# Performance work log

Hardware: AMD Instinct MI355X
Metric: run time of the kernel (lower is better)

The kernel has to match this reference:

```python
import jax, jax.numpy as jnp
import numpy as np

MODES1, MODES2 = 32, 32

def fht_matrix(N):
    # Exact linear-operator form of the repo's recursive fht1d (N must be a power of two,
    # which it is here, so the pad/truncate branch never triggers).
    if N == 1:
        return np.ones((1, 1), np.float32)
    M = fht_matrix(N // 2)
    k = np.arange(N // 2)
    cas = (np.cos(2 * np.pi * k / N) + np.sin(2 * np.pi * k / N)).astype(np.float32)[:, None]
    E = np.zeros((N // 2, N), np.float32); E[:, 0::2] = M   # even-index sub-transform
    O = np.zeros((N // 2, N), np.float32); O[:, 1::2] = M   # odd-index sub-transform
    return np.concatenate([E + cas * O, E - cas * O], axis=0)

def dht2(x, M1, M2):
    # apply the (pseudo-)Hartley transform along dims 2 then 3: X[k,l] = sum_{h,w} M1[k,h] M2[l,w] x[h,w]
    return jnp.einsum('bchw,kh,lw->bckl', x, M1, M2)

def neg_freq(a):
    # index map k -> (-k mod m) on the last two dims (flip then roll by 1)
    return jnp.roll(jnp.flip(a, axis=(-2, -1)), shift=(1, 1), axis=(-2, -1))

def compl_mul2d(x1, x2):
    x1n = neg_freq(x1)
    x2n = neg_freq(x2)
    return 0.5 * (jnp.einsum('bixy,ioxy->boxy', x1, x2)
                  - jnp.einsum('bixy,ioxy->boxy', x1n, x2n)
                  + jnp.einsum('bixy,ioxy->boxy', x1, x2n)
                  + jnp.einsum('bixy,ioxy->boxy', x1n, x2))

def setup_inputs() -> dict:
    key = jax.random.key(0)
    k1, k2 = jax.random.split(key)
    B, Cin, Cout, S = 32, 64, 64, 128
    x = jax.random.normal(k1, (B, Cin, S, S), jnp.float32)
    scale = 1.0 / (Cin * Cout)
    weights1 = scale * jax.random.uniform(k2, (Cin, Cout, MODES1, MODES2), jnp.float32)
    return {"x": x, "weights1": weights1}

def reference(x, weights1):
    B, Cin, S1, S2 = x.shape
    Cout = weights1.shape[1]
    M1 = jnp.asarray(fht_matrix(S1))
    M2 = jnp.asarray(fht_matrix(S2))
    x_ht = dht2(x, M1, M2)                                        # [B,Cin,S1,S2]
    block = compl_mul2d(x_ht[:, :, :MODES1, :MODES2], weights1)   # [B,Cout,m1,m2]
    out_ht = jnp.zeros((B, Cout, S1, S2), x.dtype).at[:, :, :MODES1, :MODES2].set(block)
    # idht = dht / (S1*S2)
    return dht2(out_ht, M1, M2) / (S1 * S2)
```

## Files before the change

### kernel.cpp

```cpp
#include <hip/hip_runtime.h>
#include <math.h>


#define SS   128
#define MD   32
#define NBAT 32
#define CI   64
#define CO   64

#define TWO_PI 6.2831853071795864769

typedef __attribute__((ext_vector_type(8))) short bf16x8;
typedef __attribute__((ext_vector_type(4))) float f32x4;

static const size_t OFF_XH   = 32768;
static const size_t OFF_XHT  = 32768 + 2097152;
static const size_t OFF_WT   = 32768 + 2 * 2097152;
static const size_t OFF_BLKT = OFF_XH;
static const size_t OFF_BLK  = OFF_XHT;
static const size_t OFF_MFH  = OFF_WT + 4194304;
static const size_t OFF_MFL  = OFF_MFH + 8192;

__device__ inline float m_entry(int k, int n) {
    float prod = 1.f;
    int kk = k, nn = n;
    for (int Nj = SS; Nj > 1; Nj >>= 1) {
        int half = Nj >> 1;
        int k1 = kk & (half - 1);
        if (nn & 1) {
            double ang = (TWO_PI / (double)Nj) * (double)k1;
            float cas = (float)(cos(ang) + sin(ang));
            prod *= (kk < half) ? cas : -cas;
        }
        kk = k1;
        nn >>= 1;
    }
    return prod;
}

__device__ inline unsigned short f2bf(float f) {
    unsigned u = __float_as_uint(f);
    return (unsigned short)((u + 0x7FFF + ((u >> 16) & 1)) >> 16);
}
__device__ inline float bf2f(unsigned short h) {
    return __uint_as_float((unsigned)h << 16);
}
__device__ inline void split2(float a, float b, unsigned& hi, unsigned& lo) {
    unsigned short ah = f2bf(a), bh = f2bf(b);
    hi = (unsigned)ah | ((unsigned)bh << 16);
    lo = (unsigned)f2bf(a - bf2f(ah)) | ((unsigned)f2bf(b - bf2f(bh)) << 16);
}
__device__ inline void fsplit2(float a, float b, unsigned& hi, unsigned& lo) {
    unsigned ua = __float_as_uint(a), ub = __float_as_uint(b);
    unsigned ha = (ua + 0x8000u) & 0xFFFF0000u;
    unsigned hb = (ub + 0x8000u) & 0xFFFF0000u;
    float la = a - __uint_as_float(ha);
    float lb = b - __uint_as_float(hb);
    hi = (ha >> 16) | hb;
    lo = (__float_as_uint(la) >> 16) | (__float_as_uint(lb) & 0xFFFF0000u);
}
__device__ inline bf16x8 pack4(unsigned a, unsigned b, unsigned c, unsigned d) {
    union { unsigned u[4]; bf16x8 v; } w;
    w.u[0] = a; w.u[1] = b; w.u[2] = c; w.u[3] = d;
    return w.v;
}

__global__ __launch_bounds__(256) void k_prep(const float* __restrict__ wgt,
                                              float* __restrict__ Wt,
                                              unsigned short* __restrict__ MFH,
                                              unsigned short* __restrict__ MFL) {
    const int bid = blockIdx.x;
    const int t   = threadIdx.x;
    if (bid >= 4096) {
        int idx2 = (bid - 4096) * 256 + t;
        int j    = idx2 & 7;
        int lane = (idx2 >> 3) & 63;
        int s    = (idx2 >> 9) & 3;
        int tt   = idx2 >> 11;
        int kq   = tt * 16 + (lane & 15);
        int nq   = s * 32 + ((lane >> 4) << 3) + j;
        float f  = m_entry(kq, nq);
        unsigned short hi = f2bf(f);
        MFH[idx2] = hi;
        MFL[idx2] = f2bf(f - bf2f(hi));
        return;
    }
    __shared__ float tile[32][33];
    const int mt  = bid & 31;
    const int iot = bid >> 5;
    const int tx = t & 31;
    const int ty = t >> 5;
#pragma unroll
    for (int j = 0; j < 4; ++j) {
        int r = ty + 8 * j;
        tile[r][tx] = wgt[(iot * 32 + r) * 1024 + mt * 32 + tx];
    }
    __syncthreads();
#pragma unroll
    for (int j = 0; j < 4; ++j) {
        int r = ty + 8 * j;
        Wt[(mt * 32 + r) * 4096 + iot * 32 + tx] = tile[tx][r];
    }
}

__global__ __launch_bounds__(256, 3) void k_fwd4(const float* __restrict__ x,
                                                 const unsigned short* __restrict__ MFH,
                                                 const unsigned short* __restrict__ MFL,
                                                 float* __restrict__ Xh) {
    const int bc = blockIdx.x;
    const float* xp = x + (size_t)bc * 16384;
    const int t = threadIdx.x;
    const int lane = t & 63, wid = t >> 6;
    const int l15 = lane & 15, g = lane >> 4;

    __shared__ unsigned short Ybf[2][32 * 136];

    const int hbase = wid * 32;
    const int ra = (hbase + l15) * 128 + g * 8;
    const int rb = (hbase + 16 + l15) * 128 + g * 8;

    float4 xall[4][2][2];
#pragma unroll
    for (int s = 0; s < 4; ++s) {
        xall[s][0][0] = *(const float4*)(xp + ra + s * 32);
        xall[s][0][1] = *(const float4*)(xp + ra + s * 32 + 4);
        xall[s][1][0] = *(const float4*)(xp + rb + s * 32);
        xall[s][1][1] = *(const float4*)(xp + rb + s * 32 + 4);
    }

    f32x4 acc[2][2] = {};

#pragma unroll
    for (int s = 0; s < 4; ++s) {
        bf16x8 Bh[2], Bl[2];
#pragma unroll
        for (int lt = 0; lt < 2; ++lt) {
            const int bidx = (lt * 4 + s) * 64 + lane;
            Bh[lt] = ((const bf16x8*)MFH)[bidx];
            Bl[lt] = ((const bf16x8*)MFL)[bidx];
        }
#pragma unroll
        for (int hh = 0; hh < 2; ++hh) {
            const float4 v0 = xall[s][hh][0];
            const float4 v1 = xall[s][hh][1];
            unsigned h0, l0, h1, l1, h2, l2, h3, l3;
            fsplit2(v0.x, v0.y, h0, l0);
            fsplit2(v0.z, v0.w, h1, l1);
            fsplit2(v1.x, v1.y, h2, l2);
            fsplit2(v1.z, v1.w, h3, l3);
            const bf16x8 Ah = pack4(h0, h1, h2, h3);
            const bf16x8 Al = pack4(l0, l1, l2, l3);
#pragma unroll
            for (int lt = 0; lt < 2; ++lt) {
                acc[hh][lt] = __builtin_amdgcn_mfma_f32_16x16x32_bf16(Ah, Bh[lt], acc[hh][lt], 0, 0, 0);
                acc[hh][lt] = __builtin_amdgcn_mfma_f32_16x16x32_bf16(Ah, Bl[lt], acc[hh][lt], 0, 0, 0);
                acc[hh][lt] = __builtin_amdgcn_mfma_f32_16x16x32_bf16(Al, Bh[lt], acc[hh][lt], 0, 0, 0);
            }
        }
    }

#pragma unroll
    for (int hh = 0; hh < 2; ++hh) {
#pragma unroll
        for (int lt = 0; lt < 2; ++lt) {
            int lmode = lt * 16 + l15;
            int h0 = hbase + hh * 16 + g * 4;
            f32x4 v = acc[hh][lt];
            unsigned hi01, lo01, hi23, lo23;
            split2(v[0], v[1], hi01, lo01);
            split2(v[2], v[3], hi23, lo23);
            ((uint2*)&Ybf[0][0])[lmode * 34 + (h0 >> 2)] = make_uint2(hi01, hi23);
            ((uint2*)&Ybf[1][0])[lmode * 34 + (h0 >> 2)] = make_uint2(lo01, lo23);
        }
    }
    __syncthreads();

    const int kt = wid >> 1, lt2 = wid & 1;
    f32x4 z = {};
#pragma unroll
    for (int s2 = 0; s2 < 4; ++s2) {
        int aidx = (kt * 4 + s2) * 64 + lane;
        bf16x8 Ah = ((const bf16x8*)MFH)[aidx];
        bf16x8 Al = ((const bf16x8*)MFL)[aidx];
        int lmode = lt2 * 16 + l15;
        int yidx = lmode * 17 + s2 * 4 + g;
        bf16x8 Yh = ((const bf16x8*)&Ybf[0][0])[yidx];
        bf16x8 Yl = ((const bf16x8*)&Ybf[1][0])[yidx];
        z = __builtin_amdgcn_mfma_f32_16x16x32_bf16(Ah, Yh, z, 0, 0, 0);
        z = __builtin_amdgcn_mfma_f32_16x16x32_bf16(Ah, Yl, z, 0, 0, 0);
        z = __builtin_amdgcn_mfma_f32_16x16x32_bf16(Al, Yh, z, 0, 0, 0);
    }
    float* op = Xh + (size_t)bc * 1024;
#pragma unroll
    for (int r = 0; r < 4; ++r)
        op[(kt * 16 + g * 4 + r) * 32 + lt2 * 16 + l15] = z[r];
}

__global__ __launch_bounds__(256) void t_xh(const float* __restrict__ Xh,
                                            float* __restrict__ Xh_t) {
    __shared__ float tile[32][33];
    const int i  = blockIdx.x & 63;
    const int mt = blockIdx.x >> 6;
    const int tx = threadIdx.x & 31;
    const int ty = threadIdx.x >> 5;
#pragma unroll
    for (int j = 0; j < 4; ++j) {
        int b = ty + 8 * j;
        tile[b][tx] = Xh[(b * 64 + i) * 1024 + mt * 32 + tx];
    }
    __syncthreads();
#pragma unroll
    for (int j = 0; j < 4; ++j) {
        int row = ty + 8 * j;
        Xh_t[(mt * 32 + row) * 2048 + i * 32 + tx] = tile[tx][row];
    }
}

__global__ __launch_bounds__(256) void k_mix4(const float* __restrict__ Xh_t,
                                              const float* __restrict__ Wt,
                                              float* __restrict__ blk_t) {
    const int m  = blockIdx.x;
    const int xm = m >> 5, ym = m & 31;
    const int nm = (((32 - xm) & 31) << 5) | ((32 - ym) & 31);
    if (m > nm) return;
    const int t = threadIdx.x;

    __shared__ float Xs[2][64][32];

    {
        const float4* xm4 = (const float4*)(Xh_t + m * 2048);
        const float4* xn4 = (const float4*)(Xh_t + nm * 2048);
        float4* s0 = (float4*)&Xs[0][0][0];
        float4* s1 = (float4*)&Xs[1][0][0];
        s0[t]       = xm4[t];
        s0[t + 256] = xm4[t + 256];
        s1[t]       = xn4[t];
        s1[t + 256] = xn4[t + 256];
    }
    __syncthreads();

    const int o  = t & 63;
    const int bq = t >> 6;
    const float* wpm = Wt + m * 4096 + o;
    const float* wpn = Wt + nm * 4096 + o;

    float am[8], an[8];
#pragma unroll
    for (int j = 0; j < 8; ++j) { am[j] = 0.f; an[j] = 0.f; }

#pragma unroll 4
    for (int i = 0; i < 64; ++i) {
        float wm = wpm[i * 64];
        float wn = wpn[i * 64];
        float we = 0.5f * (wm + wn);
        float wo = 0.5f * (wm - wn);
        const float* xr  = &Xs[0][i][bq * 8];
        const float* xrn = &Xs[1][i][bq * 8];
#pragma unroll
        for (int j = 0; j < 8; ++j) {
            float x1  = xr[j];
            float x1n = xrn[j];
            am[j] = fmaf(x1, we, fmaf(x1n, wo, am[j]));
            an[j] = fmaf(x1n, we, fmaf(x1, -wo, an[j]));
        }
    }

    float* om = blk_t + m * 2048 + o;
    float* on = blk_t + nm * 2048 + o;
#pragma unroll
    for (int j = 0; j < 8; ++j) {
        int b = bq * 8 + j;
        om[b * 64] = am[j];
        on[b * 64] = an[j];
    }
}

__global__ __launch_bounds__(256) void t_blk(const float* __restrict__ blk_t,
                                             float* __restrict__ blk) {
    __shared__ float tile[32][33];
    const int mt  = blockIdx.x & 31;
    const int bot = blockIdx.x >> 5;
    const int tx = threadIdx.x & 31;
    const int ty = threadIdx.x >> 5;
#pragma unroll
    for (int j = 0; j < 4; ++j) {
        int r = ty + 8 * j;
        tile[r][tx] = blk_t[(mt * 32 + r) * 2048 + bot * 32 + tx];
    }
    __syncthreads();
#pragma unroll
    for (int j = 0; j < 4; ++j) {
        int r = ty + 8 * j;
        blk[(bot * 32 + r) * 1024 + mt * 32 + tx] = tile[tx][r];
    }
}

__global__ __launch_bounds__(256, 2) void k_inv2(const float* __restrict__ blk,
                                                 const unsigned short* __restrict__ MFH,
                                                 const unsigned short* __restrict__ MFL,
                                                 float* __restrict__ out) {
    const int bo = blockIdx.x;
    const int t  = threadIdx.x;
    const int lane = t & 63, wid = t >> 6;
    const int l15 = lane & 15, g = lane >> 4;

    __shared__ __align__(16) unsigned short Bst[2][32 * 40];
    __shared__ __align__(16) unsigned short Tl[2][128 * 40];

    {
        float4 v = ((const float4*)(blk + (size_t)bo * 1024))[t];
        const int h = t >> 3, l0 = (t & 7) * 4;
        float vv[4] = { v.x * (1.f / 16384.f), v.y * (1.f / 16384.f),
                        v.z * (1.f / 16384.f), v.w * (1.f / 16384.f) };
#pragma unroll
        for (int q = 0; q < 4; ++q) {
            unsigned short hi = f2bf(vv[q]);
            Bst[0][(l0 + q) * 40 + h] = hi;
            Bst[1][(l0 + q) * 40 + h] = f2bf(vv[q] - bf2f(hi));
        }
    }
    __syncthreads();

#pragma unroll
    for (int rr = 0; rr < 2; ++rr) {
        const int tt = wid * 2 + rr;
        const int aidx = (tt * 4) * 64 + lane;
        bf16x8 Ah = ((const bf16x8*)MFH)[aidx];
        bf16x8 Al = ((const bf16x8*)MFL)[aidx];
#pragma unroll
        for (int lt = 0; lt < 2; ++lt) {
            bf16x8 Bh = *(const bf16x8*)&Bst[0][(lt * 16 + l15) * 40 + g * 8];
            bf16x8 Bl = *(const bf16x8*)&Bst[1][(lt * 16 + l15) * 40 + g * 8];
            f32x4 acc = {};
            acc = __builtin_amdgcn_mfma_f32_16x16x32_bf16(Ah, Bh, acc, 0, 0, 0);
            acc = __builtin_amdgcn_mfma_f32_16x16x32_bf16(Al, Bh, acc, 0, 0, 0);
            acc = __builtin_amdgcn_mfma_f32_16x16x32_bf16(Ah, Bl, acc, 0, 0, 0);
#pragma unroll
            for (int ri = 0; ri < 4; ++ri) {
                int r = tt * 16 + g * 4 + ri;
                int l = lt * 16 + l15;
                unsigned short hi = f2bf(acc[ri]);
                Tl[0][r * 40 + l] = hi;
                Tl[1][r * 40 + l] = f2bf(acc[ri] - bf2f(hi));
            }
        }
    }
    __syncthreads();

    float* op = out + (size_t)bo * (SS * SS);
#pragma unroll
    for (int rr = 0; rr < 2; ++rr) {
        const int rt = wid * 2 + rr;
        bf16x8 Bh = *(const bf16x8*)&Tl[0][(rt * 16 + l15) * 40 + g * 8];
        bf16x8 Bl = *(const bf16x8*)&Tl[1][(rt * 16 + l15) * 40 + g * 8];
        const int r = rt * 16 + l15;
#pragma unroll
        for (int ct = 0; ct < 8; ++ct) {
            const int aidx = (ct * 4) * 64 + lane;
            bf16x8 Ah = ((const bf16x8*)MFH)[aidx];
            bf16x8 Al = ((const bf16x8*)MFL)[aidx];
            f32x4 acc = {};
            acc = __builtin_amdgcn_mfma_f32_16x16x32_bf16(Ah, Bh, acc, 0, 0, 0);
            acc = __builtin_amdgcn_mfma_f32_16x16x32_bf16(Al, Bh, acc, 0, 0, 0);
            acc = __builtin_amdgcn_mfma_f32_16x16x32_bf16(Ah, Bl, acc, 0, 0, 0);
            *(float4*)&op[r * SS + ct * 16 + g * 4] =
                make_float4(acc[0], acc[1], acc[2], acc[3]);
        }
    }
}

extern "C" void kernel_launch(void* const* d_in, const int* in_sizes, int n_in,
                              void* d_out, int out_size, void* d_ws, size_t ws_size,
                              hipStream_t stream) {
    const float* x   = (const float*)d_in[0];
    const float* wgt = (const float*)d_in[1];
    float* outp = (float*)d_out;
    float* ws   = (float*)d_ws;

    float* Xh    = ws + OFF_XH;
    float* Xh_t  = ws + OFF_XHT;
    float* Wt    = ws + OFF_WT;
    float* blk_t = ws + OFF_BLKT;
    float* blk   = ws + OFF_BLK;
    unsigned short* MFH = (unsigned short*)(ws + OFF_MFH);
    unsigned short* MFL = (unsigned short*)(ws + OFF_MFL);

    k_prep <<<4160, 256, 0, stream>>>(wgt, Wt, MFH, MFL);
    k_fwd4 <<<2048, 256, 0, stream>>>(x, MFH, MFL, Xh);
    t_xh   <<<2048, 256, 0, stream>>>(Xh, Xh_t);
    k_mix4 <<<1024, 256, 0, stream>>>(Xh_t, Wt, blk_t);
    t_blk  <<<2048, 256, 0, stream>>>(blk_t, blk);
    k_inv2 <<<2048, 256, 0, stream>>>(blk, MFH, MFL, outp);
}
```

Before: 108.3 us.

## Process four images per block in forward DHT with register-prefetched double buffering

```diff
diff --git a/kernel.cpp b/kernel.cpp
--- a/kernel.cpp
+++ b/kernel.cpp
@@ -103,97 +103,114 @@
     }
 }
 
-__global__ __launch_bounds__(256, 3) void k_fwd4(const float* __restrict__ x,
-                                                 const unsigned short* __restrict__ MFH,
-                                                 const unsigned short* __restrict__ MFL,
-                                                 float* __restrict__ Xh) {
-    const int bc = blockIdx.x;
-    const float* xp = x + (size_t)bc * 16384;
+__global__ __launch_bounds__(256) void k_fwd5(const float* __restrict__ x,
+                                              const unsigned short* __restrict__ MFH,
+                                              const unsigned short* __restrict__ MFL,
+                                              float* __restrict__ Xh) {
+    const int bc0 = blockIdx.x * 4;
     const int t = threadIdx.x;
     const int lane = t & 63, wid = t >> 6;
     const int l15 = lane & 15, g = lane >> 4;
 
-    __shared__ unsigned short Ybf[2][32 * 136];
+    __shared__ unsigned short Ybf[2][2][32 * 136];
 
     const int hbase = wid * 32;
     const int ra = (hbase + l15) * 128 + g * 8;
     const int rb = (hbase + 16 + l15) * 128 + g * 8;
 
-    float4 xall[4][2][2];
-#pragma unroll
-    for (int s = 0; s < 4; ++s) {
-        xall[s][0][0] = *(const float4*)(xp + ra + s * 32);
-        xall[s][0][1] = *(const float4*)(xp + ra + s * 32 + 4);
-        xall[s][1][0] = *(const float4*)(xp + rb + s * 32);
-        xall[s][1][1] = *(const float4*)(xp + rb + s * 32 + 4);
-    }
-
-    f32x4 acc[2][2] = {};
-
-#pragma unroll
-    for (int s = 0; s < 4; ++s) {
-        bf16x8 Bh[2], Bl[2];
-#pragma unroll
-        for (int lt = 0; lt < 2; ++lt) {
-            const int bidx = (lt * 4 + s) * 64 + lane;
-            Bh[lt] = ((const bf16x8*)MFH)[bidx];
-            Bl[lt] = ((const bf16x8*)MFL)[bidx];
-        }
+    float4 xa[2][4][2][2];
+
+    {
+        const float* xp = x + (size_t)bc0 * 16384;
+#pragma unroll
+        for (int s = 0; s < 4; ++s) {
+            xa[0][s][0][0] = *(const float4*)(xp + ra + s * 32);
+            xa[0][s][0][1] = *(const float4*)(xp + ra + s * 32 + 4);
+            xa[0][s][1][0] = *(const float4*)(xp + rb + s * 32);
+            xa[0][s][1][1] = *(const float4*)(xp + rb + s * 32 + 4);
+        }
+    }
+
+#pragma unroll
+    for (int p = 0; p < 4; ++p) {
+        const int cur = p & 1;
+        if (p < 3) {
+            const float* xn = x + (size_t)(bc0 + p + 1) * 16384;
+#pragma unroll
+            for (int s = 0; s < 4; ++s) {
+                xa[cur ^ 1][s][0][0] = *(const float4*)(xn + ra + s * 32);
+                xa[cur ^ 1][s][0][1] = *(const float4*)(xn + ra + s * 32 + 4);
+                xa[cur ^ 1][s][1][0] = *(const float4*)(xn + rb + s * 32);
+                xa[cur ^ 1][s][1][1] = *(const float4*)(xn + rb + s * 32 + 4);
+            }
+        }
+
+        f32x4 acc[2][2] = {};
+#pragma unroll
+        for (int s = 0; s < 4; ++s) {
+            bf16x8 Bh[2], Bl[2];
+#pragma unroll
+            for (int lt = 0; lt < 2; ++lt) {
+                const int bidx = (lt * 4 + s) * 64 + lane;
+                Bh[lt] = ((const bf16x8*)MFH)[bidx];
+                Bl[lt] = ((const bf16x8*)MFL)[bidx];
+            }
+#pragma unroll
+            for (int hh = 0; hh < 2; ++hh) {
+                const float4 v0 = xa[cur][s][hh][0];
+                const float4 v1 = xa[cur][s][hh][1];
+                unsigned h0, l0, h1, l1, h2, l2, h3, l3;
+                fsplit2(v0.x, v0.y, h0, l0);
+                fsplit2(v0.z, v0.w, h1, l1);
+                fsplit2(v1.x, v1.y, h2, l2);
+                fsplit2(v1.z, v1.w, h3, l3);
+                const bf16x8 Ah = pack4(h0, h1, h2, h3);
+                const bf16x8 Al = pack4(l0, l1, l2, l3);
+#pragma unroll
+                for (int lt = 0; lt < 2; ++lt) {
+                    acc[hh][lt] = __builtin_amdgcn_mfma_f32_16x16x32_bf16(Ah, Bh[lt], acc[hh][lt], 0, 0, 0);
+                    acc[hh][lt] = __builtin_amdgcn_mfma_f32_16x16x32_bf16(Ah, Bl[lt], acc[hh][lt], 0, 0, 0);
+                    acc[hh][lt] = __builtin_amdgcn_mfma_f32_16x16x32_bf16(Al, Bh[lt], acc[hh][lt], 0, 0, 0);
+                }
+            }
+        }
+
 #pragma unroll
         for (int hh = 0; hh < 2; ++hh) {
-            const float4 v0 = xall[s][hh][0];
-            const float4 v1 = xall[s][hh][1];
-            unsigned h0, l0, h1, l1, h2, l2, h3, l3;
-            fsplit2(v0.x, v0.y, h0, l0);
-            fsplit2(v0.z, v0.w, h1, l1);
-            fsplit2(v1.x, v1.y, h2, l2);
-            fsplit2(v1.z, v1.w, h3, l3);
-            const bf16x8 Ah = pack4(h0, h1, h2, h3);
-            const bf16x8 Al = pack4(l0, l1, l2, l3);
 #pragma unroll
             for (int lt = 0; lt < 2; ++lt) {
-                acc[hh][lt] = __builtin_amdgcn_mfma_f32_16x16x32_bf16(Ah, Bh[lt], acc[hh][lt], 0, 0, 0);
-                acc[hh][lt] = __builtin_amdgcn_mfma_f32_16x16x32_bf16(Ah, Bl[lt], acc[hh][lt], 0, 0, 0);
-                acc[hh][lt] = __builtin_amdgcn_mfma_f32_16x16x32_bf16(Al, Bh[lt], acc[hh][lt], 0, 0, 0);
+                int lmode = lt * 16 + l15;
+                int h0 = hbase + hh * 16 + g * 4;
+                f32x4 v = acc[hh][lt];
+                unsigned hi01, lo01, hi23, lo23;
+                split2(v[0], v[1], hi01, lo01);
+                split2(v[2], v[3], hi23, lo23);
+                ((uint2*)&Ybf[cur][0][0])[lmode * 34 + (h0 >> 2)] = make_uint2(hi01, hi23);
+                ((uint2*)&Ybf[cur][1][0])[lmode * 34 + (h0 >> 2)] = make_uint2(lo01, lo23);
             }
         }
-    }
-
-#pragma unroll
-    for (int hh = 0; hh < 2; ++hh) {
-#pragma unroll
-        for (int lt = 0; lt < 2; ++lt) {
-            int lmode = lt * 16 + l15;
-            int h0 = hbase + hh * 16 + g * 4;
-            f32x4 v = acc[hh][lt];
-            unsigned hi01, lo01, hi23, lo23;
-            split2(v[0], v[1], hi01, lo01);
-            split2(v[2], v[3], hi23, lo23);
-            ((uint2*)&Ybf[0][0])[lmode * 34 + (h0 >> 2)] = make_uint2(hi01, hi23);
-            ((uint2*)&Ybf[1][0])[lmode * 34 + (h0 >> 2)] = make_uint2(lo01, lo23);
-        }
-    }
-    __syncthreads();
-
-    const int kt = wid >> 1, lt2 = wid & 1;
-    f32x4 z = {};
-#pragma unroll
-    for (int s2 = 0; s2 < 4; ++s2) {
-        int aidx = (kt * 4 + s2) * 64 + lane;
-        bf16x8 Ah = ((const bf16x8*)MFH)[aidx];
-        bf16x8 Al = ((const bf16x8*)MFL)[aidx];
-        int lmode = lt2 * 16 + l15;
-        int yidx = lmode * 17 + s2 * 4 + g;
-        bf16x8 Yh = ((const bf16x8*)&Ybf[0][0])[yidx];
-        bf16x8 Yl = ((const bf16x8*)&Ybf[1][0])[yidx];
-        z = __builtin_amdgcn_mfma_f32_16x16x32_bf16(Ah, Yh, z, 0, 0, 0);
-        z = __builtin_amdgcn_mfma_f32_16x16x32_bf16(Ah, Yl, z, 0, 0, 0);
-        z = __builtin_amdgcn_mfma_f32_16x16x32_bf16(Al, Yh, z, 0, 0, 0);
-    }
-    float* op = Xh + (size_t)bc * 1024;
-#pragma unroll
-    for (int r = 0; r < 4; ++r)
-        op[(kt * 16 + g * 4 + r) * 32 + lt2 * 16 + l15] = z[r];
+        __syncthreads();
+
+        const int kt = wid >> 1, lt2 = wid & 1;
+        f32x4 z = {};
+#pragma unroll
+        for (int s2 = 0; s2 < 4; ++s2) {
+            int aidx = (kt * 4 + s2) * 64 + lane;
+            bf16x8 Ah = ((const bf16x8*)MFH)[aidx];
+            bf16x8 Al = ((const bf16x8*)MFL)[aidx];
+            int lmode = lt2 * 16 + l15;
+            int yidx = lmode * 17 + s2 * 4 + g;
+            bf16x8 Yh = ((const bf16x8*)&Ybf[cur][0][0])[yidx];
+            bf16x8 Yl = ((const bf16x8*)&Ybf[cur][1][0])[yidx];
+            z = __builtin_amdgcn_mfma_f32_16x16x32_bf16(Ah, Yh, z, 0, 0, 0);
+            z = __builtin_amdgcn_mfma_f32_16x16x32_bf16(Ah, Yl, z, 0, 0, 0);
+            z = __builtin_amdgcn_mfma_f32_16x16x32_bf16(Al, Yh, z, 0, 0, 0);
+        }
+        float* op = Xh + (size_t)(bc0 + p) * 1024;
+#pragma unroll
+        for (int r = 0; r < 4; ++r)
+            op[(kt * 16 + g * 4 + r) * 32 + lt2 * 16 + l15] = z[r];
+    }
 }
 
 __global__ __launch_bounds__(256) void t_xh(const float* __restrict__ Xh,
@@ -386,7 +403,7 @@
     unsigned short* MFL = (unsigned short*)(ws + OFF_MFL);
 
     k_prep <<<4160, 256, 0, stream>>>(wgt, Wt, MFH, MFL);
-    k_fwd4 <<<2048, 256, 0, stream>>>(x, MFH, MFL, Xh);
+    k_fwd5 <<<512, 256, 0, stream>>>(x, MFH, MFL, Xh);
     t_xh   <<<2048, 256, 0, stream>>>(Xh, Xh_t);
     k_mix4 <<<1024, 256, 0, stream>>>(Xh_t, Wt, blk_t);
     t_blk  <<<2048, 256, 0, stream>>>(blk_t, blk);
```

Measured after the change: 112.4 us. 3.8% more time.

## Stage forward-transform input through double-buffered LDS via direct global-to-LDS loads

Applied to the files above, without the earlier changes.

```diff
diff --git a/kernel.cpp b/kernel.cpp
--- a/kernel.cpp
+++ b/kernel.cpp
@@ -103,7 +103,7 @@
     }
 }
 
-__global__ __launch_bounds__(256, 3) void k_fwd4(const float* __restrict__ x,
+__global__ __launch_bounds__(256, 2) void k_fwd6(const float* __restrict__ x,
                                                  const unsigned short* __restrict__ MFH,
                                                  const unsigned short* __restrict__ MFL,
                                                  float* __restrict__ Xh) {
@@ -113,36 +113,54 @@
     const int lane = t & 63, wid = t >> 6;
     const int l15 = lane & 15, g = lane >> 4;
 
-    __shared__ unsigned short Ybf[2][32 * 136];
-
+    __shared__ __align__(16) float Pan[2][4096];
+    __shared__ __align__(16) unsigned short Ybf[2][32 * 136];
+
+    bf16x8 TBh[2][4], TBl[2][4];
+#pragma unroll
+    for (int lt = 0; lt < 2; ++lt)
+#pragma unroll
+        for (int s = 0; s < 4; ++s) {
+            const int bidx = (lt * 4 + s) * 64 + lane;
+            TBh[lt][s] = ((const bf16x8*)MFH)[bidx];
+            TBl[lt][s] = ((const bf16x8*)MFL)[bidx];
+        }
+
+    const int slot  = wid * 64 + lane;
+    const int srow  = slot >> 3, s16 = slot & 7;
+    const int sbyte0 = srow * 512 + (((s16 >> 1) ^ (srow & 3)) * 32) + (s16 & 1) * 16;
+
+#define STAGE(buf, sp)                                                         \
+    {                                                                          \
+        _Pragma("unroll")                                                      \
+        for (int j = 0; j < 4; ++j) {                                          \
+            int slot2 = j * 256 + slot;                                        \
+            int row2 = slot2 >> 3, t16 = slot2 & 7;                            \
+            const char* gp = (const char*)xp + row2 * 512 + (sp) * 128 +       \
+                             (((t16 >> 1) ^ (row2 & 3)) * 32) + (t16 & 1) * 16;\
+            char* lp = (char*)&Pan[buf][0] + j * 4096 + wid * 1024;            \
+            __builtin_amdgcn_global_load_lds(                                  \
+                (const __attribute__((address_space(1))) void*)gp,             \
+                (__attribute__((address_space(3))) void*)lp, 16, 0, 0);        \
+        }                                                                      \
+    }
+    (void)sbyte0;
+
+    f32x4 acc[2][2] = {};
     const int hbase = wid * 32;
-    const int ra = (hbase + l15) * 128 + g * 8;
-    const int rb = (hbase + 16 + l15) * 128 + g * 8;
-
-    float4 xall[4][2][2];
+
+    STAGE(0, 0);
 #pragma unroll
     for (int s = 0; s < 4; ++s) {
-        xall[s][0][0] = *(const float4*)(xp + ra + s * 32);
-        xall[s][0][1] = *(const float4*)(xp + ra + s * 32 + 4);
-        xall[s][1][0] = *(const float4*)(xp + rb + s * 32);
-        xall[s][1][1] = *(const float4*)(xp + rb + s * 32 + 4);
-    }
-
-    f32x4 acc[2][2] = {};
-
-#pragma unroll
-    for (int s = 0; s < 4; ++s) {
-        bf16x8 Bh[2], Bl[2];
-#pragma unroll
-        for (int lt = 0; lt < 2; ++lt) {
-            const int bidx = (lt * 4 + s) * 64 + lane;
-            Bh[lt] = ((const bf16x8*)MFH)[bidx];
-            Bl[lt] = ((const bf16x8*)MFL)[bidx];
-        }
+        const int cur = s & 1;
+        __syncthreads();
+        if (s < 3) STAGE(cur ^ 1, s + 1);
 #pragma unroll
         for (int hh = 0; hh < 2; ++hh) {
-            const float4 v0 = xall[s][hh][0];
-            const float4 v1 = xall[s][hh][1];
+            const int row = hbase + hh * 16 + l15;
+            const float* pr = &Pan[cur][row * 32 + ((g ^ (row & 3)) * 8)];
+            const float4 v0 = *(const float4*)pr;
+            const float4 v1 = *(const float4*)(pr + 4);
             unsigned h0, l0, h1, l1, h2, l2, h3, l3;
             fsplit2(v0.x, v0.y, h0, l0);
             fsplit2(v0.z, v0.w, h1, l1);
@@ -152,9 +170,9 @@
             const bf16x8 Al = pack4(l0, l1, l2, l3);
 #pragma unroll
             for (int lt = 0; lt < 2; ++lt) {
-                acc[hh][lt] = __builtin_amdgcn_mfma_f32_16x16x32_bf16(Ah, Bh[lt], acc[hh][lt], 0, 0, 0);
-                acc[hh][lt] = __builtin_amdgcn_mfma_f32_16x16x32_bf16(Ah, Bl[lt], acc[hh][lt], 0, 0, 0);
-                acc[hh][lt] = __builtin_amdgcn_mfma_f32_16x16x32_bf16(Al, Bh[lt], acc[hh][lt], 0, 0, 0);
+                acc[hh][lt] = __builtin_amdgcn_mfma_f32_16x16x32_bf16(Ah, TBh[lt][s], acc[hh][lt], 0, 0, 0);
+                acc[hh][lt] = __builtin_amdgcn_mfma_f32_16x16x32_bf16(Ah, TBl[lt][s], acc[hh][lt], 0, 0, 0);
+                acc[hh][lt] = __builtin_amdgcn_mfma_f32_16x16x32_bf16(Al, TBh[lt][s], acc[hh][lt], 0, 0, 0);
             }
         }
     }
@@ -194,6 +212,7 @@
 #pragma unroll
     for (int r = 0; r < 4; ++r)
         op[(kt * 16 + g * 4 + r) * 32 + lt2 * 16 + l15] = z[r];
+#undef STAGE
 }
 
 __global__ __launch_bounds__(256) void t_xh(const float* __restrict__ Xh,
@@ -386,7 +405,7 @@
     unsigned short* MFL = (unsigned short*)(ws + OFF_MFL);
 
     k_prep <<<4160, 256, 0, stream>>>(wgt, Wt, MFH, MFL);
-    k_fwd4 <<<2048, 256, 0, stream>>>(x, MFH, MFL, Xh);
+    k_fwd6 <<<2048, 256, 0, stream>>>(x, MFH, MFL, Xh);
     t_xh   <<<2048, 256, 0, stream>>>(Xh, Xh_t);
     k_mix4 <<<1024, 256, 0, stream>>>(Xh_t, Wt, blk_t);
     t_blk  <<<2048, 256, 0, stream>>>(blk_t, blk);
```

Measured after the change: 108.3 us. No clear change (-0.0%).

## Stage forward-transform input through swizzled LDS with coalesced panel loads

Applied to the files above, without the earlier changes.

```diff
diff --git a/kernel.cpp b/kernel.cpp
--- a/kernel.cpp
+++ b/kernel.cpp
@@ -59,11 +59,8 @@
     hi = (ha >> 16) | hb;
     lo = (__float_as_uint(la) >> 16) | (__float_as_uint(lb) & 0xFFFF0000u);
 }
-__device__ inline bf16x8 pack4(unsigned a, unsigned b, unsigned c, unsigned d) {
-    union { unsigned u[4]; bf16x8 v; } w;
-    w.u[0] = a; w.u[1] = b; w.u[2] = c; w.u[3] = d;
-    return w.v;
-}
+
+#define PIN4(v) asm volatile("" :: "v"((v).x), "v"((v).y), "v"((v).z), "v"((v).w))
 
 __global__ __launch_bounds__(256) void k_prep(const float* __restrict__ wgt,
                                               float* __restrict__ Wt,
@@ -103,74 +100,81 @@
     }
 }
 
-__global__ __launch_bounds__(256, 3) void k_fwd4(const float* __restrict__ x,
+__global__ __launch_bounds__(256, 4) void k_fwd8(const float* __restrict__ x,
                                                  const unsigned short* __restrict__ MFH,
                                                  const unsigned short* __restrict__ MFL,
                                                  float* __restrict__ Xh) {
     const int bc = blockIdx.x;
-    const float* xp = x + (size_t)bc * 16384;
+    const float4* xp4 = (const float4*)(x + (size_t)bc * 16384);
     const int t = threadIdx.x;
     const int lane = t & 63, wid = t >> 6;
     const int l15 = lane & 15, g = lane >> 4;
 
-    __shared__ unsigned short Ybf[2][32 * 136];
-
-    const int hbase = wid * 32;
-    const int ra = (hbase + l15) * 128 + g * 8;
-    const int rb = (hbase + 16 + l15) * 128 + g * 8;
-
-    float4 xall[4][2][2];
-#pragma unroll
-    for (int s = 0; s < 4; ++s) {
-        xall[s][0][0] = *(const float4*)(xp + ra + s * 32);
-        xall[s][0][1] = *(const float4*)(xp + ra + s * 32 + 4);
-        xall[s][1][0] = *(const float4*)(xp + rb + s * 32);
-        xall[s][1][1] = *(const float4*)(xp + rb + s * 32 + 4);
-    }
+    __shared__ __align__(16) unsigned short smem[16384];
+    unsigned short* Hs  = smem;
+    unsigned short* Ls  = smem + 8192;
+    unsigned short* Yb0 = smem;
+    unsigned short* Yb1 = smem + 4352;
 
     f32x4 acc[2][2] = {};
 
 #pragma unroll
-    for (int s = 0; s < 4; ++s) {
-        bf16x8 Bh[2], Bl[2];
-#pragma unroll
-        for (int lt = 0; lt < 2; ++lt) {
-            const int bidx = (lt * 4 + s) * 64 + lane;
-            Bh[lt] = ((const bf16x8*)MFH)[bidx];
-            Bl[lt] = ((const bf16x8*)MFL)[bidx];
-        }
-#pragma unroll
-        for (int hh = 0; hh < 2; ++hh) {
-            const float4 v0 = xall[s][hh][0];
-            const float4 v1 = xall[s][hh][1];
-            unsigned h0, l0, h1, l1, h2, l2, h3, l3;
-            fsplit2(v0.x, v0.y, h0, l0);
-            fsplit2(v0.z, v0.w, h1, l1);
-            fsplit2(v1.x, v1.y, h2, l2);
-            fsplit2(v1.z, v1.w, h3, l3);
-            const bf16x8 Ah = pack4(h0, h1, h2, h3);
-            const bf16x8 Al = pack4(l0, l1, l2, l3);
+    for (int pan = 0; pan < 2; ++pan) {
+        float4 v[8];
+#pragma unroll
+        for (int j = 0; j < 8; ++j)
+            v[j] = xp4[pan * 2048 + t + 256 * j];
+#pragma unroll
+        for (int j = 0; j < 8; ++j) PIN4(v[j]);
+        __syncthreads();
+#pragma unroll
+        for (int j = 0; j < 8; ++j) {
+            int q = t + 256 * j;
+            int rp = q >> 5, c16 = q & 31;
+            int cp = (((c16 >> 1) ^ (rp & 7)) << 1) | (c16 & 1);
+            unsigned h01, l01, h23, l23;
+            fsplit2(v[j].x, v[j].y, h01, l01);
+            fsplit2(v[j].z, v[j].w, h23, l23);
+            ((uint2*)Hs)[rp * 32 + cp] = make_uint2(h01, h23);
+            ((uint2*)Ls)[rp * 32 + cp] = make_uint2(l01, l23);
+        }
+        __syncthreads();
+
+        const int rp2 = wid * 16 + l15;
+#pragma unroll
+        for (int s = 0; s < 4; ++s) {
+            bf16x8 Bh[2], Bl[2];
 #pragma unroll
             for (int lt = 0; lt < 2; ++lt) {
-                acc[hh][lt] = __builtin_amdgcn_mfma_f32_16x16x32_bf16(Ah, Bh[lt], acc[hh][lt], 0, 0, 0);
-                acc[hh][lt] = __builtin_amdgcn_mfma_f32_16x16x32_bf16(Ah, Bl[lt], acc[hh][lt], 0, 0, 0);
-                acc[hh][lt] = __builtin_amdgcn_mfma_f32_16x16x32_bf16(Al, Bh[lt], acc[hh][lt], 0, 0, 0);
+                const int bidx = (lt * 4 + s) * 64 + lane;
+                Bh[lt] = ((const bf16x8*)MFH)[bidx];
+                Bl[lt] = ((const bf16x8*)MFL)[bidx];
             }
-        }
-    }
+            const int cidx = (s * 4 + g) ^ (rp2 & 7);
+            bf16x8 Ah = ((const bf16x8*)Hs)[rp2 * 16 + cidx];
+            bf16x8 Al = ((const bf16x8*)Ls)[rp2 * 16 + cidx];
+#pragma unroll
+            for (int lt = 0; lt < 2; ++lt) {
+                acc[pan][lt] = __builtin_amdgcn_mfma_f32_16x16x32_bf16(Ah, Bh[lt], acc[pan][lt], 0, 0, 0);
+                acc[pan][lt] = __builtin_amdgcn_mfma_f32_16x16x32_bf16(Ah, Bl[lt], acc[pan][lt], 0, 0, 0);
+                acc[pan][lt] = __builtin_amdgcn_mfma_f32_16x16x32_bf16(Al, Bh[lt], acc[pan][lt], 0, 0, 0);
+            }
+        }
+    }
+    __syncthreads();
 
 #pragma unroll
     for (int hh = 0; hh < 2; ++hh) {
 #pragma unroll
         for (int lt = 0; lt < 2; ++lt) {
             int lmode = lt * 16 + l15;
-            int h0 = hbase + hh * 16 + g * 4;
-            f32x4 v = acc[hh][lt];
+            int h0 = hh * 64 + wid * 16 + g * 4;
+            f32x4 vv = acc[hh][lt];
             unsigned hi01, lo01, hi23, lo23;
-            split2(v[0], v[1], hi01, lo01);
-            split2(v[2], v[3], hi23, lo23);
-            ((uint2*)&Ybf[0][0])[lmode * 34 + (h0 >> 2)] = make_uint2(hi01, hi23);
-            ((uint2*)&Ybf[1][0])[lmode * 34 + (h0 >> 2)] = make_uint2(lo01, lo23);
+            split2(vv[0], vv[1], hi01, lo01);
+            split2(vv[2], vv[3], hi23, lo23);
+            ((uint2*)Yb0)[lmode * 34 + (h0 >> 2)] = make_uint2(hi01, hi23);
+            ((uint2*)Yb1)[lmode * 34 + (h0 >> 2)] = make_uint2(lo01, lo23);
         }
     }
     __syncthreads();
@@ -184,8 +188,8 @@
         bf16x8 Al = ((const bf16x8*)MFL)[aidx];
         int lmode = lt2 * 16 + l15;
         int yidx = lmode * 17 + s2 * 4 + g;
-        bf16x8 Yh = ((const bf16x8*)&Ybf[0][0])[yidx];
-        bf16x8 Yl = ((const bf16x8*)&Ybf[1][0])[yidx];
+        bf16x8 Yh = ((const bf16x8*)Yb0)[yidx];
+        bf16x8 Yl = ((const bf16x8*)Yb1)[yidx];
         z = __builtin_amdgcn_mfma_f32_16x16x32_bf16(Ah, Yh, z, 0, 0, 0);
         z = __builtin_amdgcn_mfma_f32_16x16x32_bf16(Ah, Yl, z, 0, 0, 0);
         z = __builtin_amdgcn_mfma_f32_16x16x32_bf16(Al, Yh, z, 0, 0, 0);
@@ -386,7 +390,7 @@
     unsigned short* MFL = (unsigned short*)(ws + OFF_MFL);
 
     k_prep <<<4160, 256, 0, stream>>>(wgt, Wt, MFH, MFL);
-    k_fwd4 <<<2048, 256, 0, stream>>>(x, MFH, MFL, Xh);
+    k_fwd8 <<<2048, 256, 0, stream>>>(x, MFH, MFL, Xh);
     t_xh   <<<2048, 256, 0, stream>>>(Xh, Xh_t);
     k_mix4 <<<1024, 256, 0, stream>>>(Xh_t, Wt, blk_t);
     t_blk  <<<2048, 256, 0, stream>>>(blk_t, blk);
```

New measurement: 109.7 us. No clear change (+1.3%).
